# Optimization experiments

Measured on AMD Instinct MI355X. Metric: run time of the kernel, lower is better.

## Reference

```python
import jax, jax.numpy as jnp
import numpy as np

T, B, E, H = 256, 8, 512, 32
EXP = 512            # number of expanded (periodic-image) keys
SMOOTH = 20.0        # smooth_factor


def setup_inputs() -> dict:
    key = jax.random.key(0)
    ks = jax.random.split(key, 12)
    s = 1.0 / np.sqrt(E)
    return {
        "query": jax.random.normal(ks[0], (T, B, E), dtype=jnp.float32),
        "outcell_index": jax.random.randint(ks[1], (B, EXP), 0, T),
        "expand_mask": jax.random.bernoulli(ks[2], 0.1, (B, EXP)),
        "key_padding_mask": jax.random.bernoulli(ks[3], 0.1, (B, T)),
        "local_attention_weight": jax.random.uniform(ks[4], (B, T, T + EXP), dtype=jnp.float32),
        "Wq": jax.random.normal(ks[5], (E, E), dtype=jnp.float32) * s,
        "bq": jnp.zeros((E,), dtype=jnp.float32),
        "Wk": jax.random.normal(ks[6], (E, E), dtype=jnp.float32) * s,   # k_bias=False
        "Wv": jax.random.normal(ks[7], (E, E), dtype=jnp.float32) * s,
        "bv": jnp.zeros((E,), dtype=jnp.float32),
        "Wo": jax.random.normal(ks[8], (E, E), dtype=jnp.float32) * s,
        "bo": jnp.zeros((E,), dtype=jnp.float32),
    }


def reference(query, outcell_index, expand_mask, key_padding_mask,
              local_attention_weight, Wq, bq, Wk, Wv, bv, Wo, bo):
    t, b, e = query.shape
    hd = e // H
    # QKV projections (torch Linear: y = x @ W.T + b)
    q = jnp.einsum('tbe,fe->tbf', query, Wq) + bq
    k = jnp.einsum('tbe,fe->tbf', query, Wk)          # no k bias
    v = jnp.einsum('tbe,fe->tbf', query, Wv) + bv
    # PBC gather-expand K/V along the time axis
    oc = outcell_index.T[:, :, None]                  # [EXP, B, 1]
    k = jnp.concatenate([k, jnp.take_along_axis(k, oc, axis=0)], axis=0)  # [S,B,E]
    v = jnp.concatenate([v, jnp.take_along_axis(v, oc, axis=0)], axis=0)
    s_len = k.shape[0]
    # [len, B, E] -> [B, H, len, hd]
    qh = q.reshape(t, b, H, hd).transpose(1, 2, 0, 3)
    kh = k.reshape(s_len, b, H, hd).transpose(1, 2, 0, 3)
    vh = v.reshape(s_len, b, H, hd).transpose(1, 2, 0, 3)
    # NOTE: forward() never applies self.scaling in this path (faithful)
    scores = jnp.einsum('bhtd,bhsd->bhts', qh, kh)    # [B,H,T,S]
    law = local_attention_weight[:, None]             # [B,1,T,S]
    scores = (scores + SMOOTH) * law - SMOOTH         # smooth softmax
    kpm = jnp.concatenate([key_padding_mask, expand_mask], axis=1)  # [B,S]
    scores = jnp.where(kpm[:, None, None, :], -jnp.inf, scores)
    probs = jax.nn.softmax(scores, axis=-1)
    probs = probs * law                               # post-softmax reweight
    attn = jnp.einsum('bhts,bhsd->bhtd', probs, vh)   # [B,H,T,hd]
    attn = attn.transpose(2, 0, 1, 3).reshape(t, b, e)
    return jnp.einsum('tbe,fe->tbf', attn, Wo) + bo
```

## Files before the change

kernel.cpp:

```cpp
#include <hip/hip_runtime.h>
#include <stdint.h>

#define T_ 256
#define B_ 8
#define E_ 512
#define H_ 32
#define HD_ 16
#define EXP_ 512
#define S_ 768
#define M_ 2048
#define SMOOTH_ 20.0f
#define PSTR 40
#define VSTR 800
#define OSTR 20

typedef __attribute__((ext_vector_type(8)))  short bf16x8;
typedef __attribute__((ext_vector_type(4)))  float f32x4;
typedef __attribute__((ext_vector_type(16))) float f32x16;

__device__ __forceinline__ unsigned int pk2(float a, float b)
{
    unsigned int ua = __float_as_uint(a);
    ua = ua + 0x7FFFu + ((ua >> 16) & 1u);
    unsigned int ub = __float_as_uint(b);
    ub = ub + 0x7FFFu + ((ub >> 16) & 1u);
    return (ua >> 16) | (ub & 0xFFFF0000u);
}
__device__ __forceinline__ ushort bf1(float a)
{
    unsigned int u = __float_as_uint(a);
    u = u + 0x7FFFu + ((u >> 16) & 1u);
    return (ushort)(u >> 16);
}

union U16 { uint4 u; bf16x8 v; };

__global__ __launch_bounds__(256)
void conv_kernel(const float* __restrict__ X,
                 const float* __restrict__ Wq, const float* __restrict__ Wk,
                 const float* __restrict__ Wv, const float* __restrict__ Wo,
                 ushort* __restrict__ Xb, ushort* __restrict__ Wb)
{
    const int seg = blockIdx.x >> 6;
    const int blk = blockIdx.x & 63;
    const float* src;
    ushort* dst;
    if (seg < 4) { src = X + (size_t)seg * 262144; dst = Xb + (size_t)seg * 262144; }
    else {
        const float* ws_[4] = {Wq, Wk, Wv, Wo};
        src = ws_[seg - 4];
        dst = Wb + (size_t)(seg - 4) * 262144;
    }
    const int base = blk * 4096 + threadIdx.x * 16;
    float4 f0 = *(const float4*)&src[base + 0];
    float4 f1 = *(const float4*)&src[base + 4];
    float4 f2 = *(const float4*)&src[base + 8];
    float4 f3 = *(const float4*)&src[base + 12];
    *(uint4*)&dst[base + 0] = make_uint4(pk2(f0.x, f0.y), pk2(f0.z, f0.w),
                                         pk2(f1.x, f1.y), pk2(f1.z, f1.w));
    *(uint4*)&dst[base + 8] = make_uint4(pk2(f2.x, f2.y), pk2(f2.z, f2.w),
                                         pk2(f3.x, f3.y), pk2(f3.z, f3.w));
}

__device__ __forceinline__ void mfma_gemm_body_bf(const ushort* __restrict__ Xr,
                                                  int xstep,
                                                  const ushort* __restrict__ Wr,
                                                  int wstep,
                                                  f32x4 acc[2][2],
                                                  ushort* As, ushort* Bs)
{
    const int tid  = threadIdx.x;
    const int lrow = tid >> 2;
    const int kq   = tid & 3;
    const int l    = tid & 63;
    const int w    = tid >> 6;
    const int wm   = w & 1;
    const int wn   = w >> 1;
    const int lq   = l >> 4;
    const int ln   = l & 15;

    ushort* Aw = &As[lrow * 72 + kq * 16];
    ushort* Bw = &Bs[lrow * 72 + kq * 16];

    uint4 a0 = *(const uint4*)&Xr[0];
    uint4 a1 = *(const uint4*)&Xr[8];
    uint4 b0 = *(const uint4*)&Wr[0];
    uint4 b1 = *(const uint4*)&Wr[8];

    for (int it = 0; it < E_ / 64; ++it) {
        __syncthreads();
        *(uint4*)&Aw[0] = a0;
        *(uint4*)&Aw[8] = a1;
        *(uint4*)&Bw[0] = b0;
        *(uint4*)&Bw[8] = b1;
        __syncthreads();
        if (it < E_ / 64 - 1) {
            Xr += xstep; Wr += wstep;
            a0 = *(const uint4*)&Xr[0];
            a1 = *(const uint4*)&Xr[8];
            b0 = *(const uint4*)&Wr[0];
            b1 = *(const uint4*)&Wr[8];
        }
#pragma unroll
        for (int kb = 0; kb < 2; ++kb) {
            bf16x8 af0 = *(const bf16x8*)&As[(32 * wm + ln) * 72 + 32 * kb + lq * 8];
            bf16x8 af1 = *(const bf16x8*)&As[(32 * wm + 16 + ln) * 72 + 32 * kb + lq * 8];
            bf16x8 bf0 = *(const bf16x8*)&Bs[(32 * wn + ln) * 72 + 32 * kb + lq * 8];
            bf16x8 bf1 = *(const bf16x8*)&Bs[(32 * wn + 16 + ln) * 72 + 32 * kb + lq * 8];
            acc[0][0] = __builtin_amdgcn_mfma_f32_16x16x32_bf16(af0, bf0, acc[0][0], 0, 0, 0);
            acc[0][1] = __builtin_amdgcn_mfma_f32_16x16x32_bf16(af0, bf1, acc[0][1], 0, 0, 0);
            acc[1][0] = __builtin_amdgcn_mfma_f32_16x16x32_bf16(af1, bf0, acc[1][0], 0, 0, 0);
            acc[1][1] = __builtin_amdgcn_mfma_f32_16x16x32_bf16(af1, bf1, acc[1][1], 0, 0, 0);
        }
    }
}

__global__ __launch_bounds__(256)
void qkv_gemm(const ushort* __restrict__ Xb, const ushort* __restrict__ Wb,
              const float* __restrict__ bq, const float* __restrict__ bv,
              ushort* __restrict__ Qb, ushort* __restrict__ Kb,
              ushort* __restrict__ Vb)
{
    __shared__ __align__(16) ushort AsBs[2 * 64 * 72];
    ushort* As = AsBs;
    ushort* Bs = AsBs + 64 * 72;

    const int z = blockIdx.z;
    const ushort* W    = Wb + (size_t)z * 262144;
    const float*  bias = (z == 0) ? bq : (z == 2 ? bv : nullptr);
    ushort* dst        = (z == 0) ? Qb : (z == 1 ? Kb : Vb);

    const int m0 = blockIdx.y * 64;
    const int n0 = blockIdx.x * 64;

    f32x4 acc[2][2];
#pragma unroll
    for (int i = 0; i < 2; ++i)
#pragma unroll
        for (int j = 0; j < 2; ++j)
            acc[i][j] = (f32x4){0.f, 0.f, 0.f, 0.f};

    const int tid  = threadIdx.x;
    const int lrow = tid >> 2;
    const int kq   = tid & 3;
    mfma_gemm_body_bf(&Xb[(size_t)(m0 + lrow) * E_ + kq * 16], 64,
                      &W[(size_t)(n0 + lrow) * E_ + kq * 16], 64,
                      acc, As, Bs);

    const int l  = tid & 63;
    const int w  = tid >> 6;
    const int wm = w & 1;
    const int wn = w >> 1;
    const int lq = l >> 4;
    const int ln = l & 15;

    const float b0_ = bias ? bias[n0 + 32 * wn + ln]      : 0.f;
    const float b1_ = bias ? bias[n0 + 32 * wn + 16 + ln] : 0.f;

    __syncthreads();
    ushort* Ls = As;
#pragma unroll
    for (int j = 0; j < 2; ++j) {
        const float bb = j ? b1_ : b0_;
#pragma unroll
        for (int i = 0; i < 2; ++i)
#pragma unroll
            for (int r = 0; r < 4; ++r)
                Ls[(32 * wm + 16 * i + lq * 4 + r) * 72 + 32 * wn + 16 * j + ln] =
                    bf1(acc[i][j][r] + bb);
    }
    __syncthreads();

    {
        const int lm = tid & 63;
        const int hh = tid >> 6;
        uint4 f0 = *(const uint4*)&Ls[lm * 72 + hh * 16];
        uint4 f1 = *(const uint4*)&Ls[lm * 72 + hh * 16 + 8];
        const int m = m0 + lm;
        const int t = m >> 3;
        const int b = m & 7;
        const int h = (n0 >> 4) + hh;
        ushort* dp = &dst[(((size_t)(b * H_ + h)) * T_ + t) * HD_];
        *(uint4*)&dp[0] = f0;
        *(uint4*)&dp[8] = f1;
    }
}

__global__ __launch_bounds__(256)
void out_gemm(const ushort* __restrict__ Ab, const ushort* __restrict__ Wob,
              const float* __restrict__ bo, float* __restrict__ dst)
{
    __shared__ __align__(16) ushort AsBs[2 * 64 * 72];
    ushort* As = AsBs;
    ushort* Bs = AsBs + 64 * 72;

    const int m0 = blockIdx.y * 64;
    const int n0 = blockIdx.x * 64;

    f32x4 acc[2][2];
#pragma unroll
    for (int i = 0; i < 2; ++i)
#pragma unroll
        for (int j = 0; j < 2; ++j)
            acc[i][j] = (f32x4){0.f, 0.f, 0.f, 0.f};

    const int tid  = threadIdx.x;
    const int lrow = tid >> 2;
    const int kq   = tid & 3;
    const int m    = m0 + lrow;
    const int t    = m >> 3;
    const int b    = m & 7;
    mfma_gemm_body_bf(&Ab[(((size_t)(b * H_ + kq)) * T_ + t) * HD_], 4 * T_ * HD_,
                      &Wob[(size_t)(n0 + lrow) * E_ + kq * 16], 64,
                      acc, As, Bs);

    const int l  = tid & 63;
    const int w  = tid >> 6;
    const int wm = w & 1;
    const int wn = w >> 1;
    const int lq = l >> 4;
    const int ln = l & 15;

    const float bo0 = bo[n0 + 32 * wn + ln];
    const float bo1 = bo[n0 + 32 * wn + 16 + ln];

    __syncthreads();
    float* Lf = (float*)AsBs;
#pragma unroll
    for (int j = 0; j < 2; ++j) {
        const float bb = j ? bo1 : bo0;
#pragma unroll
        for (int i = 0; i < 2; ++i)
#pragma unroll
            for (int r = 0; r < 4; ++r)
                Lf[(32 * wm + 16 * i + lq * 4 + r) * 68 + 32 * wn + 16 * j + ln] =
                    acc[i][j][r] + bb;
    }
    __syncthreads();

    {
        const int lm = tid & 63;
        const int hh = tid >> 6;
        float* dp = &dst[(size_t)(m0 + lm) * E_ + n0 + hh * 16];
#pragma unroll
        for (int c = 0; c < 4; ++c) {
            float4 v = *(const float4*)&Lf[lm * 68 + hh * 16 + c * 4];
            *(float4*)&dp[c * 4] = v;
        }
    }
}

__device__ __forceinline__ void scat8(ushort* d, uint4 u)
{
    d[0 * VSTR] = (ushort)(u.x);  d[1 * VSTR] = (ushort)(u.x >> 16);
    d[2 * VSTR] = (ushort)(u.y);  d[3 * VSTR] = (ushort)(u.y >> 16);
    d[4 * VSTR] = (ushort)(u.z);  d[5 * VSTR] = (ushort)(u.z >> 16);
    d[6 * VSTR] = (ushort)(u.w);  d[7 * VSTR] = (ushort)(u.w >> 16);
}

__global__ __launch_bounds__(512)
void attn_kernel(const ushort* __restrict__ Qb, const ushort* __restrict__ Kb,
                 const ushort* __restrict__ Vb, const float* __restrict__ LAW,
                 const int* __restrict__ kpm, const int* __restrict__ em,
                 const int* __restrict__ oc, ushort* __restrict__ Ab)
{
    __shared__ __align__(16) ushort Ks[S_ * HD_];
    __shared__ __align__(16) ushort Vt[HD_ * VSTR];
    __shared__ __align__(16) float  msf[S_];
    __shared__ __align__(16) ushort Pb[8][32 * PSTR];
    __shared__ __align__(16) float  Zpart[2][128];

    float*  Obuf = (float*)Ks;
    ushort* Ob   = (ushort*)Vt;

    const int tid    = threadIdx.x;
    const int blk    = blockIdx.x;
    const int bh     = blk >> 1;
    const int thalf  = blk & 1;
    const int b      = bh >> 5;
    const int h      = bh & 31;

    ((uint4*)Ks)[tid] = ((const uint4*)&Kb[(size_t)bh * T_ * HD_])[tid];
    {
        const int t    = tid >> 1;
        const int half = tid & 1;
        uint4 v = *(const uint4*)&Vb[((size_t)bh * T_ + t) * HD_ + half * 8];
        scat8(&Vt[half * 8 * VSTR + t], v);
    }
    {
        const int j   = tid;
        const int src = oc[b * EXP_ + j];
        const uint4* kr = (const uint4*)&Kb[((size_t)bh * T_ + src) * HD_];
        *(uint4*)&Ks[(T_ + j) * HD_ + 0] = kr[0];
        *(uint4*)&Ks[(T_ + j) * HD_ + 8] = kr[1];
        const uint4* vr = (const uint4*)&Vb[((size_t)bh * T_ + src) * HD_];
        scat8(&Vt[T_ + j], vr[0]);
        scat8(&Vt[8 * VSTR + T_ + j], vr[1]);
    }
    {
        const int s = tid;
        const int m = (s < T_) ? kpm[b * T_ + s] : em[b * EXP_ + (s - T_)];
        msf[s] = m ? 0.f : 1.f;
        if (tid < 256) {
            const int s2 = 512 + tid;
            msf[s2] = em[b * EXP_ + (s2 - T_)] ? 0.f : 1.f;
        }
    }

    const int w      = tid >> 6;
    const int l      = tid & 63;
    const int slane  = l & 31;
    const int khalf  = l >> 5;
    const int wt     = w & 3;
    const int sh     = w >> 2;
    const int tbase  = thalf * 128 + wt * 32;
    bf16x8 qf = *(const bf16x8*)&Qb[((size_t)bh * T_ + tbase + slane) * HD_ + khalf * 8];

    __syncthreads();

    const f32x16 zero16 = {0.f,0.f,0.f,0.f,0.f,0.f,0.f,0.f,
                           0.f,0.f,0.f,0.f,0.f,0.f,0.f,0.f};
    f32x4 o0 = {0.f, 0.f, 0.f, 0.f};
    f32x4 o1 = {0.f, 0.f, 0.f, 0.f};
    float zacc[16];
#pragma unroll
    for (int r = 0; r < 16; ++r) zacc[r] = 0.f;

    const float* lawb = &LAW[((size_t)b * T_ + tbase + khalf * 4) * S_ + slane];
    ushort* pw = &Pb[w][slane];
    const int tl = l & 15;
    const int kg = l >> 4;

    for (int i = sh * 12; i < sh * 12 + 12; ++i) {
        bf16x8 kf = *(const bf16x8*)&Ks[(i * 32 + slane) * HD_ + khalf * 8];

        float lw[16];
        const float* lp = lawb + i * 32;
#pragma unroll
        for (int r = 0; r < 16; ++r)
            lw[r] = lp[(size_t)((r & 3) + 8 * (r >> 2)) * S_];

        f32x16 sc = __builtin_amdgcn_mfma_f32_32x32x16_bf16(qf, kf, zero16, 0, 0, 0);
        const float mval = msf[i * 32 + slane];

#pragma unroll
        for (int r = 0; r < 16; ++r) {
            const float x = (sc[r] + SMOOTH_) * lw[r] - SMOOTH_;
            const float e = mval * __expf(x - 50.f);
            zacc[r] += e;
            pw[((r & 3) + 8 * (r >> 2) + 4 * khalf) * PSTR] = bf1(e * lw[r]);
        }

        bf16x8 vf = *(const bf16x8*)&Vt[tl * VSTR + i * 32 + kg * 8];
        {
            const ushort* pr0 = &Pb[w][(0 * 16 + tl) * PSTR + kg * 8];
            U16 u;
            uint2 a0 = *(const uint2*)pr0;
            uint2 a1 = *(const uint2*)(pr0 + 4);
            u.u = make_uint4(a0.x, a0.y, a1.x, a1.y);
            o0 = __builtin_amdgcn_mfma_f32_16x16x32_bf16(vf, u.v, o0, 0, 0, 0);
            const ushort* pr1 = &Pb[w][(1 * 16 + tl) * PSTR + kg * 8];
            uint2 b0 = *(const uint2*)pr1;
            uint2 b1 = *(const uint2*)(pr1 + 4);
            u.u = make_uint4(b0.x, b0.y, b1.x, b1.y);
            o1 = __builtin_amdgcn_mfma_f32_16x16x32_bf16(vf, u.v, o1, 0, 0, 0);
        }
    }

#pragma unroll
    for (int m = 1; m < 32; m <<= 1) {
#pragma unroll
        for (int r = 0; r < 16; ++r)
            zacc[r] += __shfl_xor(zacc[r], m);
    }

    __syncthreads();

    if (l == 0 || l == 32) {
#pragma unroll
        for (int r = 0; r < 16; ++r)
            Zpart[sh][wt * 32 + (r & 3) + 8 * (r >> 2) + 4 * khalf] = zacc[r];
    }
    if (sh == 1) {
#pragma unroll
        for (int th = 0; th < 2; ++th) {
            const f32x4 o = th ? o1 : o0;
            *(float4*)&Obuf[((wt * 2 + th) * 16 + tl) * OSTR + kg * 4] =
                make_float4(o[0], o[1], o[2], o[3]);
        }
    }
    __syncthreads();

    if (sh == 0) {
#pragma unroll
        for (int th = 0; th < 2; ++th) {
            const int trow = wt * 32 + th * 16 + tl;
            const float Zt  = Zpart[0][trow] + Zpart[1][trow];
            const float inv = (Zt > 0.f) ? 1.f / Zt : 0.f;
            float4 po = *(const float4*)&Obuf[((wt * 2 + th) * 16 + tl) * OSTR + kg * 4];
            const f32x4 o = th ? o1 : o0;
            float ov[4] = {(o[0] + po.x) * inv, (o[1] + po.y) * inv,
                           (o[2] + po.z) * inv, (o[3] + po.w) * inv};
            *(uint*)&Ob[trow * 16 + kg * 4]     = pk2(ov[0], ov[1]);
            *(uint*)&Ob[trow * 16 + kg * 4 + 2] = pk2(ov[2], ov[3]);
        }
    }
    __syncthreads();

    if (tid < 256) {
        ushort* dp = &Ab[(((size_t)(b * H_ + h)) * T_ + thalf * 128) * HD_];
        *(uint4*)&dp[tid * 8] = *(const uint4*)&Ob[tid * 8];
    }
}

extern "C" void kernel_launch(void* const* d_in, const int* in_sizes, int n_in,
                              void* d_out, int out_size, void* d_ws, size_t ws_size,
                              hipStream_t stream)
{
    const float* query = (const float*)d_in[0];
    const int*   oc    = (const int*)d_in[1];
    const int*   em    = (const int*)d_in[2];
    const int*   kpm   = (const int*)d_in[3];
    const float* law   = (const float*)d_in[4];
    const float* Wq    = (const float*)d_in[5];
    const float* bq    = (const float*)d_in[6];
    const float* Wk    = (const float*)d_in[7];
    const float* Wv    = (const float*)d_in[8];
    const float* bv    = (const float*)d_in[9];
    const float* Wo    = (const float*)d_in[10];
    const float* bo    = (const float*)d_in[11];
    float* out = (float*)d_out;

    ushort* Xb  = (ushort*)d_ws;
    ushort* Wb  = Xb  + (size_t)1048576;
    ushort* Qb  = Wb  + (size_t)1048576;
    ushort* Kb  = Qb  + (size_t)1048576;
    ushort* Vb  = Kb  + (size_t)1048576;
    ushort* Ab  = Vb  + (size_t)1048576;

    conv_kernel<<<512, 256, 0, stream>>>(query, Wq, Wk, Wv, Wo, Xb, Wb);

    dim3 gq(E_ / 64, M_ / 64, 3);
    qkv_gemm<<<gq, 256, 0, stream>>>(Xb, Wb, bq, bv, Qb, Kb, Vb);

    attn_kernel<<<B_ * H_ * 2, 512, 0, stream>>>(Qb, Kb, Vb, law, kpm, em, oc, Ab);

    dim3 go(E_ / 64, M_ / 64, 1);
    out_gemm<<<go, 256, 0, stream>>>(Ab, Wb + (size_t)3 * 262144, bo, out);
}
```

Baseline: 126.5 us.

## Fuse fp32-to-bf16 conversion into GEMM loaders and fold softmax mask into exp2

Removes the separate conversion kernel: the QKV and output GEMMs now load fp32 inputs and weights directly and round to bf16 while staging into shared memory. In attention, the multiplicative mask and fixed offset become an additive bias feeding a single fma-chain into exp2, and bf16 rounding drops round-to-nearest-even for a cheaper round-half-up. This saves one launch and a round trip of bf16 copies through memory, at the cost of twice the global load bytes per GEMM tile and repeated conversion of X and W across blocks.

After: 130.8 us. 1.03x slower.

```diff
diff --git a/kernel.cpp b/kernel.cpp
--- a/kernel.cpp
+++ b/kernel.cpp
@@ -13,18 +13,17 @@
 #define PSTR 40
 #define VSTR 800
 #define OSTR 20
+#define LOG2E_ 1.44269504f
+#define MB0_  (-100.988655f)
 
 typedef __attribute__((ext_vector_type(8)))  short bf16x8;
 typedef __attribute__((ext_vector_type(4)))  float f32x4;
 typedef __attribute__((ext_vector_type(16))) float f32x16;
 
-__device__ __forceinline__ unsigned int pk2(float a, float b)
-{
-    unsigned int ua = __float_as_uint(a);
-    ua = ua + 0x7FFFu + ((ua >> 16) & 1u);
-    unsigned int ub = __float_as_uint(b);
-    ub = ub + 0x7FFFu + ((ub >> 16) & 1u);
-    return (ua >> 16) | (ub & 0xFFFF0000u);
+__device__ __forceinline__ unsigned int pku(float a, float b)
+{
+    return ((__float_as_uint(a) + 0x8000u) >> 16) |
+           ((__float_as_uint(b) + 0x8000u) & 0xFFFF0000u);
 }
 __device__ __forceinline__ ushort bf1(float a)
 {
@@ -35,39 +34,11 @@
 
 union U16 { uint4 u; bf16x8 v; };
 
-__global__ __launch_bounds__(256)
-void conv_kernel(const float* __restrict__ X,
-                 const float* __restrict__ Wq, const float* __restrict__ Wk,
-                 const float* __restrict__ Wv, const float* __restrict__ Wo,
-                 ushort* __restrict__ Xb, ushort* __restrict__ Wb)
-{
-    const int seg = blockIdx.x >> 6;
-    const int blk = blockIdx.x & 63;
-    const float* src;
-    ushort* dst;
-    if (seg < 4) { src = X + (size_t)seg * 262144; dst = Xb + (size_t)seg * 262144; }
-    else {
-        const float* ws_[4] = {Wq, Wk, Wv, Wo};
-        src = ws_[seg - 4];
-        dst = Wb + (size_t)(seg - 4) * 262144;
-    }
-    const int base = blk * 4096 + threadIdx.x * 16;
-    float4 f0 = *(const float4*)&src[base + 0];
-    float4 f1 = *(const float4*)&src[base + 4];
-    float4 f2 = *(const float4*)&src[base + 8];
-    float4 f3 = *(const float4*)&src[base + 12];
-    *(uint4*)&dst[base + 0] = make_uint4(pk2(f0.x, f0.y), pk2(f0.z, f0.w),
-                                         pk2(f1.x, f1.y), pk2(f1.z, f1.w));
-    *(uint4*)&dst[base + 8] = make_uint4(pk2(f2.x, f2.y), pk2(f2.z, f2.w),
-                                         pk2(f3.x, f3.y), pk2(f3.z, f3.w));
-}
-
-__device__ __forceinline__ void mfma_gemm_body_bf(const ushort* __restrict__ Xr,
-                                                  int xstep,
-                                                  const ushort* __restrict__ Wr,
-                                                  int wstep,
-                                                  f32x4 acc[2][2],
-                                                  ushort* As, ushort* Bs)
+template<bool AF, bool BF>
+__device__ __forceinline__ void gemm_body(const void* __restrict__ Xp, int xstep,
+                                          const void* __restrict__ Wp, int wstep,
+                                          f32x4 acc[2][2],
+                                          ushort* As, ushort* Bs)
 {
     const int tid  = threadIdx.x;
     const int lrow = tid >> 2;
@@ -82,24 +53,65 @@
     ushort* Aw = &As[lrow * 72 + kq * 16];
     ushort* Bw = &Bs[lrow * 72 + kq * 16];
 
-    uint4 a0 = *(const uint4*)&Xr[0];
-    uint4 a1 = *(const uint4*)&Xr[8];
-    uint4 b0 = *(const uint4*)&Wr[0];
-    uint4 b1 = *(const uint4*)&Wr[8];
+    const float*  Xf = (const float*)Xp;
+    const ushort* Xh = (const ushort*)Xp;
+    const float*  Wf = (const float*)Wp;
+    const ushort* Wh = (const ushort*)Wp;
+
+    float4 fa0, fa1, fa2, fa3, fb0, fb1, fb2, fb3;
+    uint4  ha0, ha1, hb0, hb1;
+
+    if (AF) {
+        fa0 = *(const float4*)&Xf[0];  fa1 = *(const float4*)&Xf[4];
+        fa2 = *(const float4*)&Xf[8];  fa3 = *(const float4*)&Xf[12];
+    } else {
+        ha0 = *(const uint4*)&Xh[0];   ha1 = *(const uint4*)&Xh[8];
+    }
+    if (BF) {
+        fb0 = *(const float4*)&Wf[0];  fb1 = *(const float4*)&Wf[4];
+        fb2 = *(const float4*)&Wf[8];  fb3 = *(const float4*)&Wf[12];
+    } else {
+        hb0 = *(const uint4*)&Wh[0];   hb1 = *(const uint4*)&Wh[8];
+    }
 
     for (int it = 0; it < E_ / 64; ++it) {
         __syncthreads();
-        *(uint4*)&Aw[0] = a0;
-        *(uint4*)&Aw[8] = a1;
-        *(uint4*)&Bw[0] = b0;
-        *(uint4*)&Bw[8] = b1;
+        if (AF) {
+            *(uint4*)&Aw[0] = make_uint4(pku(fa0.x, fa0.y), pku(fa0.z, fa0.w),
+                                         pku(fa1.x, fa1.y), pku(fa1.z, fa1.w));
+            *(uint4*)&Aw[8] = make_uint4(pku(fa2.x, fa2.y), pku(fa2.z, fa2.w),
+                                         pku(fa3.x, fa3.y), pku(fa3.z, fa3.w));
+        } else {
+            *(uint4*)&Aw[0] = ha0;
+            *(uint4*)&Aw[8] = ha1;
+        }
+        if (BF) {
+            *(uint4*)&Bw[0] = make_uint4(pku(fb0.x, fb0.y), pku(fb0.z, fb0.w),
+                                         pku(fb1.x, fb1.y), pku(fb1.z, fb1.w));
+            *(uint4*)&Bw[8] = make_uint4(pku(fb2.x, fb2.y), pku(fb2.z, fb2.w),
+                                         pku(fb3.x, fb3.y), pku(fb3.z, fb3.w));
+        } else {
+            *(uint4*)&Bw[0] = hb0;
+            *(uint4*)&Bw[8] = hb1;
+        }
         __syncthreads();
         if (it < E_ / 64 - 1) {
-            Xr += xstep; Wr += wstep;
-            a0 = *(const uint4*)&Xr[0];
-            a1 = *(const uint4*)&Xr[8];
-            b0 = *(const uint4*)&Wr[0];
-            b1 = *(const uint4*)&Wr[8];
+            if (AF) {
+                Xf += xstep;
+                fa0 = *(const float4*)&Xf[0];  fa1 = *(const float4*)&Xf[4];
+                fa2 = *(const float4*)&Xf[8];  fa3 = *(const float4*)&Xf[12];
+            } else {
+                Xh += xstep;
+                ha0 = *(const uint4*)&Xh[0];   ha1 = *(const uint4*)&Xh[8];
+            }
+            if (BF) {
+                Wf += wstep;
+                fb0 = *(const float4*)&Wf[0];  fb1 = *(const float4*)&Wf[4];
+                fb2 = *(const float4*)&Wf[8];  fb3 = *(const float4*)&Wf[12];
+            } else {
+                Wh += wstep;
+                hb0 = *(const uint4*)&Wh[0];   hb1 = *(const uint4*)&Wh[8];
+            }
         }
 #pragma unroll
         for (int kb = 0; kb < 2; ++kb) {
@@ -116,7 +128,9 @@
 }
 
 __global__ __launch_bounds__(256)
-void qkv_gemm(const ushort* __restrict__ Xb, const ushort* __restrict__ Wb,
+void qkv_gemm(const float* __restrict__ X,
+              const float* __restrict__ Wq, const float* __restrict__ Wk,
+              const float* __restrict__ Wv,
               const float* __restrict__ bq, const float* __restrict__ bv,
               ushort* __restrict__ Qb, ushort* __restrict__ Kb,
               ushort* __restrict__ Vb)
@@ -126,8 +140,8 @@
     ushort* Bs = AsBs + 64 * 72;
 
     const int z = blockIdx.z;
-    const ushort* W    = Wb + (size_t)z * 262144;
-    const float*  bias = (z == 0) ? bq : (z == 2 ? bv : nullptr);
+    const float* W     = (z == 0) ? Wq : (z == 1 ? Wk : Wv);
+    const float* bias  = (z == 0) ? bq : (z == 2 ? bv : nullptr);
     ushort* dst        = (z == 0) ? Qb : (z == 1 ? Kb : Vb);
 
     const int m0 = blockIdx.y * 64;
@@ -143,9 +157,9 @@
     const int tid  = threadIdx.x;
     const int lrow = tid >> 2;
     const int kq   = tid & 3;
-    mfma_gemm_body_bf(&Xb[(size_t)(m0 + lrow) * E_ + kq * 16], 64,
-                      &W[(size_t)(n0 + lrow) * E_ + kq * 16], 64,
-                      acc, As, Bs);
+    gemm_body<true, true>(&X[(size_t)(m0 + lrow) * E_ + kq * 16], 64,
+                          &W[(size_t)(n0 + lrow) * E_ + kq * 16], 64,
+                          acc, As, Bs);
 
     const int l  = tid & 63;
     const int w  = tid >> 6;
@@ -187,7 +201,7 @@
 }
 
 __global__ __launch_bounds__(256)
-void out_gemm(const ushort* __restrict__ Ab, const ushort* __restrict__ Wob,
+void out_gemm(const ushort* __restrict__ Ab, const float* __restrict__ Wo,
               const float* __restrict__ bo, float* __restrict__ dst)
 {
     __shared__ __align__(16) ushort AsBs[2 * 64 * 72];
@@ -210,9 +224,9 @@
     const int m    = m0 + lrow;
     const int t    = m >> 3;
     const int b    = m & 7;
-    mfma_gemm_body_bf(&Ab[(((size_t)(b * H_ + kq)) * T_ + t) * HD_], 4 * T_ * HD_,
-                      &Wob[(size_t)(n0 + lrow) * E_ + kq * 16], 64,
-                      acc, As, Bs);
+    gemm_body<false, true>(&Ab[(((size_t)(b * H_ + kq)) * T_ + t) * HD_], 4 * T_ * HD_,
+                           &Wo[(size_t)(n0 + lrow) * E_ + kq * 16], 64,
+                           acc, As, Bs);
 
     const int l  = tid & 63;
     const int w  = tid >> 6;
@@ -300,10 +314,10 @@
     {
         const int s = tid;
         const int m = (s < T_) ? kpm[b * T_ + s] : em[b * EXP_ + (s - T_)];
-        msf[s] = m ? 0.f : 1.f;
+        msf[s] = m ? -1.0e5f : MB0_;
         if (tid < 256) {
             const int s2 = 512 + tid;
-            msf[s2] = em[b * EXP_ + (s2 - T_)] ? 0.f : 1.f;
+            msf[s2] = em[b * EXP_ + (s2 - T_)] ? -1.0e5f : MB0_;
         }
     }
 
@@ -341,14 +355,18 @@
             lw[r] = lp[(size_t)((r & 3) + 8 * (r >> 2)) * S_];
 
         f32x16 sc = __builtin_amdgcn_mfma_f32_32x32x16_bf16(qf, kf, zero16, 0, 0, 0);
-        const float mval = msf[i * 32 + slane];
+        const float mb = msf[i * 32 + slane];
 
 #pragma unroll
         for (int r = 0; r < 16; ++r) {
-            const float x = (sc[r] + SMOOTH_) * lw[r] - SMOOTH_;
-            const float e = mval * __expf(x - 50.f);
+            const float lwK = lw[r] * LOG2E_;
+            const float arg = __builtin_fmaf(sc[r], lwK,
+                              __builtin_fmaf(lwK, SMOOTH_, mb));
+            const float e = __builtin_amdgcn_exp2f(arg);
             zacc[r] += e;
-            pw[((r & 3) + 8 * (r >> 2) + 4 * khalf) * PSTR] = bf1(e * lw[r]);
+            const float p = e * lw[r];
+            pw[((r & 3) + 8 * (r >> 2) + 4 * khalf) * PSTR] =
+                (ushort)((__float_as_uint(p) + 0x8000u) >> 16);
         }
 
         bf16x8 vf = *(const bf16x8*)&Vt[tl * VSTR + i * 32 + kg * 8];
@@ -401,8 +419,8 @@
             const f32x4 o = th ? o1 : o0;
             float ov[4] = {(o[0] + po.x) * inv, (o[1] + po.y) * inv,
                            (o[2] + po.z) * inv, (o[3] + po.w) * inv};
-            *(uint*)&Ob[trow * 16 + kg * 4]     = pk2(ov[0], ov[1]);
-            *(uint*)&Ob[trow * 16 + kg * 4 + 2] = pk2(ov[2], ov[3]);
+            *(uint*)&Ob[trow * 16 + kg * 4]     = pku(ov[0], ov[1]);
+            *(uint*)&Ob[trow * 16 + kg * 4 + 2] = pku(ov[2], ov[3]);
         }
     }
     __syncthreads();
@@ -431,20 +449,16 @@
     const float* bo    = (const float*)d_in[11];
     float* out = (float*)d_out;
 
-    ushort* Xb  = (ushort*)d_ws;
-    ushort* Wb  = Xb  + (size_t)1048576;
-    ushort* Qb  = Wb  + (size_t)1048576;
-    ushort* Kb  = Qb  + (size_t)1048576;
-    ushort* Vb  = Kb  + (size_t)1048576;
-    ushort* Ab  = Vb  + (size_t)1048576;
-
-    conv_kernel<<<512, 256, 0, stream>>>(query, Wq, Wk, Wv, Wo, Xb, Wb);
+    ushort* Qb = (ushort*)d_ws;
+    ushort* Kb = Qb + (size_t)1048576;
+    ushort* Vb = Kb + (size_t)1048576;
+    ushort* Ab = Vb + (size_t)1048576;
 
     dim3 gq(E_ / 64, M_ / 64, 3);
-    qkv_gemm<<<gq, 256, 0, stream>>>(Xb, Wb, bq, bv, Qb, Kb, Vb);
+    qkv_gemm<<<gq, 256, 0, stream>>>(query, Wq, Wk, Wv, bq, bv, Qb, Kb, Vb);
 
     attn_kernel<<<B_ * H_ * 2, 512, 0, stream>>>(Qb, Kb, Vb, law, kpm, em, oc, Ab);
 
     dim3 go(E_ / 64, M_ / 64, 1);
-    out_gemm<<<go, 256, 0, stream>>>(Ab, Wb + (size_t)3 * 262144, bo, out);
-}
+    out_gemm<<<go, 256, 0, stream>>>(Ab, Wo, bo, out);
+}
```
